# Kernel tuning notes

Measured on AMD Instinct MI355X. Metric: run time of the kernel, lower is better.

## Reference

```python
import jax, jax.numpy as jnp
import numpy as np

B, L, H, C = 1, 512, 1024, 2


def setup_inputs() -> dict:
    key = jax.random.key(0)
    k1, k2, k3 = jax.random.split(key, 3)
    lm_output = jax.random.normal(k1, (B, L, H), dtype=jnp.float32)
    # torch Linear weight layout: [out_features, in_features]
    W1 = jax.random.normal(k2, (H, 2 * H), dtype=jnp.float32) * 0.02
    b1 = jnp.zeros((H,), dtype=jnp.float32)
    W2 = jax.random.normal(k3, (C, H), dtype=jnp.float32) * 0.02
    b2 = jnp.zeros((C,), dtype=jnp.float32)
    return {"lm_output": lm_output, "W1": W1, "b1": b1, "W2": W2, "b2": b2}


def reference(lm_output, W1, b1, W2, b2):
    # pair_emb[b,i,j] = concat(lm_output[b,j], lm_output[b,i])
    # Linear(concat(a,b)) decomposes: split W1 into the halves acting on each part.
    Wa = W1[:, :H]  # acts on lm_output_a (the j / column token)
    Wb = W1[:, H:]  # acts on lm_output_b (the i / row token)
    a_proj = jnp.einsum('blh,oh->blo', lm_output, Wa)  # [B,L,H]
    b_proj = jnp.einsum('blh,oh->blo', lm_output, Wb)  # [B,L,H]
    # hidden[b,i,j] = tanh(a_proj[b,j] + b_proj[b,i] + b1)   -> [B,L,L,H]
    hidden = jnp.tanh(a_proj[:, None, :, :] + b_proj[:, :, None, :] + b1)
    # Dropout is identity at inference time.
    logits = jnp.einsum('bijh,ch->bijc', hidden, W2) + b2  # [B,L,L,C]
    logits = (logits + jnp.swapaxes(logits, 1, 2)) / 2.0
    return logits
```

## Files before the change

kernel.cpp:

```cpp
#include <hip/hip_runtime.h>
#include <hip/hip_bf16.h>

#define HH 1024
#define LL 512

typedef __attribute__((ext_vector_type(8))) short bf16x8;
typedef __attribute__((ext_vector_type(4))) float f32x4;

static constexpr float C_EXP = 2.8853900817779268f;

static __device__ __forceinline__ uint4 pack8(float4 a, float4 b) {
    union { uint4 u; __hip_bfloat162 h[4]; } r;
    r.h[0] = __float22bfloat162_rn(make_float2(a.x, a.y));
    r.h[1] = __float22bfloat162_rn(make_float2(a.z, a.w));
    r.h[2] = __float22bfloat162_rn(make_float2(b.x, b.y));
    r.h[3] = __float22bfloat162_rn(make_float2(b.z, b.w));
    return r.u;
}

__global__ __launch_bounds__(256) void proj_mfma_kernel(
    const float* __restrict__ lm, const float* __restrict__ W1,
    const float* __restrict__ b1, float* __restrict__ Ea, float* __restrict__ Eb)
{
    __shared__ ushort As[32][72];
    __shared__ ushort Bs[64][72];

    const int tid  = threadIdx.x;
    const int lane = tid & 63;
    const int w    = tid >> 6;
    const int mbase = blockIdx.y * 32;
    const int nbase = blockIdx.x * 64;
    const int wm = (w & 1) * 16;
    const int wn = (w >> 1) * 32;

    const int sel  = nbase >> 10;
    const int nrow = nbase & 1023;

    f32x4 acc0 = {0.f, 0.f, 0.f, 0.f};
    f32x4 acc1 = {0.f, 0.f, 0.f, 0.f};

    const int srow = tid >> 3;
    const int sc8  = (tid & 7) * 8;

    const int mrow = lane & 15;
    const int q8   = (lane >> 4) * 8;

    for (int kb = 0; kb < HH; kb += 64) {
        __syncthreads();
        {
            const float* pa = &lm[(mbase + srow) * HH + kb + sc8];
            *(uint4*)&As[srow][sc8] = pack8(*(const float4*)pa, *(const float4*)(pa + 4));
            const float* pb0 = &W1[(nrow + srow) * 2048 + sel * 1024 + kb + sc8];
            *(uint4*)&Bs[srow][sc8] = pack8(*(const float4*)pb0, *(const float4*)(pb0 + 4));
            const float* pb1 = &W1[(nrow + srow + 32) * 2048 + sel * 1024 + kb + sc8];
            *(uint4*)&Bs[srow + 32][sc8] = pack8(*(const float4*)pb1, *(const float4*)(pb1 + 4));
        }
        __syncthreads();

#pragma unroll
        for (int s = 0; s < 2; ++s) {
            const bf16x8 a  = *(const bf16x8*)&As[wm + mrow][s * 32 + q8];
            const bf16x8 b0 = *(const bf16x8*)&Bs[wn + mrow][s * 32 + q8];
            const bf16x8 bf = *(const bf16x8*)&Bs[wn + 16 + mrow][s * 32 + q8];
            acc0 = __builtin_amdgcn_mfma_f32_16x16x32_bf16(a, b0, acc0, 0, 0, 0);
            acc1 = __builtin_amdgcn_mfma_f32_16x16x32_bf16(a, bf, acc1, 0, 0, 0);
        }
    }

    const int col = lane & 15;
    const int rq  = (lane >> 4) * 4;
#pragma unroll
    for (int t = 0; t < 2; ++t) {
        const f32x4 acc = t ? acc1 : acc0;
        const int n_g = nbase + wn + t * 16 + col;
        const int m0  = mbase + wm + rq;
        if (n_g < HH) {
            const float bb = b1[n_g];
#pragma unroll
            for (int r = 0; r < 4; ++r)
                Ea[(m0 + r) * HH + n_g] = __builtin_amdgcn_exp2f(C_EXP * (acc[r] + bb));
        } else {
#pragma unroll
            for (int r = 0; r < 4; ++r)
                Eb[(m0 + r) * HH + (n_g - HH)] = __builtin_amdgcn_exp2f(C_EXP * acc[r]);
        }
    }
}

__global__ __launch_bounds__(256, 4) void pair_kernel(
    const float* __restrict__ Ea, const float* __restrict__ Eb,
    const float* __restrict__ W2, const float* __restrict__ b2,
    float* __restrict__ out)
{
    __shared__ float a_s[32][132];
    __shared__ float b_s[32][132];
    __shared__ float w0_s[256], w1_s[256];
    __shared__ float s_red[2];

    const int tid   = threadIdx.x;
    const int tx    = tid & 15;
    const int ty    = tid >> 4;
    const int jbase = blockIdx.x * 32;
    const int ibase = blockIdx.y * 32;
    const int k0    = blockIdx.z * 256;

    if (tid < 128) {
        const int c = tid >> 6, q = tid & 63;
        const float4 v = *(const float4*)&W2[c * HH + k0 + q * 4];
        ((float4*)(c ? w1_s : w0_s))[q] =
            make_float4(-2.f * v.x, -2.f * v.y, -2.f * v.z, -2.f * v.w);
    }
    if (tid < 128) {
        const int c = tid >> 6, l = tid & 63;
        const float* ws = c ? w1_s : w0_s;
        float s = ws[l] + ws[l + 64] + ws[l + 128] + ws[l + 192];
#pragma unroll
        for (int off = 32; off; off >>= 1) s += __shfl_down(s, off, 64);
        if (l == 0) s_red[c] = s;
    }

    float acc[2][2][2] = {};

    for (int kb = 0; kb < 256; kb += 128) {
        __syncthreads();
        int p = tid;
#pragma unroll
        for (int it = 0; it < 8; ++it, p += 256) {
            const int row = p >> 5;
            const int c4  = p & 31;
            if (row < 32)
                *(float4*)&a_s[row][c4 * 4] =
                    *(const float4*)&Ea[(jbase + row) * HH + k0 + kb + c4 * 4];
            else
                *(float4*)&b_s[row - 32][c4 * 4] =
                    *(const float4*)&Eb[(ibase + row - 32) * HH + k0 + kb + c4 * 4];
        }
        __syncthreads();

#pragma unroll 4
        for (int h4 = 0; h4 < 32; ++h4) {
            const float4 ea0 = *(const float4*)&a_s[tx][h4 * 4];
            const float4 ea1 = *(const float4*)&a_s[tx + 16][h4 * 4];
            const float4 eb0 = *(const float4*)&b_s[ty][h4 * 4];
            const float4 eb1 = *(const float4*)&b_s[ty + 16][h4 * 4];
            const float4 w0  = *(const float4*)&w0_s[kb + h4 * 4];
            const float4 w1  = *(const float4*)&w1_s[kb + h4 * 4];

#define DO_H(EA0, EA1, EB0, EB1, W0V, W1V)                            \
            {                                                         \
                const float d00 = __builtin_fmaf((EB0), (EA0), 1.f);  \
                const float d01 = __builtin_fmaf((EB0), (EA1), 1.f);  \
                const float d10 = __builtin_fmaf((EB1), (EA0), 1.f);  \
                const float d11 = __builtin_fmaf((EB1), (EA1), 1.f);  \
                const float p0 = d00 * d01, p1 = d10 * d11;           \
                const float R  = __builtin_amdgcn_rcpf(p0 * p1);      \
                const float q0 = R * p1, q1 = R * p0;                 \
                const float r00 = q0 * d01, r01 = q0 * d00;           \
                const float r10 = q1 * d11, r11 = q1 * d10;           \
                acc[0][0][0] = __builtin_fmaf(r00, (W0V), acc[0][0][0]); \
                acc[0][0][1] = __builtin_fmaf(r00, (W1V), acc[0][0][1]); \
                acc[0][1][0] = __builtin_fmaf(r01, (W0V), acc[0][1][0]); \
                acc[0][1][1] = __builtin_fmaf(r01, (W1V), acc[0][1][1]); \
                acc[1][0][0] = __builtin_fmaf(r10, (W0V), acc[1][0][0]); \
                acc[1][0][1] = __builtin_fmaf(r10, (W1V), acc[1][0][1]); \
                acc[1][1][0] = __builtin_fmaf(r11, (W0V), acc[1][1][0]); \
                acc[1][1][1] = __builtin_fmaf(r11, (W1V), acc[1][1][1]); \
            }
            DO_H(ea0.x, ea1.x, eb0.x, eb1.x, w0.x, w1.x)
            DO_H(ea0.y, ea1.y, eb0.y, eb1.y, w0.y, w1.y)
            DO_H(ea0.z, ea1.z, eb0.z, eb1.z, w0.z, w1.z)
            DO_H(ea0.w, ea1.w, eb0.w, eb1.w, w0.w, w1.w)
#undef DO_H
        }
    }

    const float sc0 = -0.25f * s_red[0];
    const float sc1 = -0.25f * s_red[1];
    const float bb0 = (blockIdx.z == 0) ? 0.5f * b2[0] : 0.f;
    const float bb1 = (blockIdx.z == 0) ? 0.5f * b2[1] : 0.f;

#pragma unroll
    for (int ii = 0; ii < 2; ++ii) {
#pragma unroll
        for (int jj = 0; jj < 2; ++jj) {
            const int i = ibase + ty + ii * 16;
            const int j = jbase + tx + jj * 16;
            const float v0 = 0.5f * acc[ii][jj][0] + sc0 + bb0;
            const float v1 = 0.5f * acc[ii][jj][1] + sc1 + bb1;
            atomicAdd(&out[(i * LL + j) * 2 + 0], v0);
            atomicAdd(&out[(i * LL + j) * 2 + 1], v1);
            atomicAdd(&out[(j * LL + i) * 2 + 0], v0);
            atomicAdd(&out[(j * LL + i) * 2 + 1], v1);
        }
    }
}

extern "C" void kernel_launch(void* const* d_in, const int* in_sizes, int n_in,
                              void* d_out, int out_size, void* d_ws, size_t ws_size,
                              hipStream_t stream)
{
    const float* lm = (const float*)d_in[0];
    const float* W1 = (const float*)d_in[1];
    const float* b1 = (const float*)d_in[2];
    const float* W2 = (const float*)d_in[3];
    const float* b2 = (const float*)d_in[4];
    float* out = (float*)d_out;

    float* Ea = (float*)d_ws;
    float* Eb = Ea + (size_t)LL * HH;

    hipMemsetAsync(d_out, 0, (size_t)LL * LL * 2 * sizeof(float), stream);
    proj_mfma_kernel<<<dim3(32, 16), 256, 0, stream>>>(lm, W1, b1, Ea, Eb);
    pair_kernel<<<dim3(16, 16, 4), 256, 0, stream>>>(Ea, Eb, W2, b2, out);
}
```

Baseline: 157.3 us.

## Exploit output symmetry with upper-triangle tiles and deterministic split-K combine

Result: faster. 137.1 us (-12.9%).

```diff
diff --git a/kernel.cpp b/kernel.cpp
--- a/kernel.cpp
+++ b/kernel.cpp
@@ -3,6 +3,8 @@
 
 #define HH 1024
 #define LL 512
+#define NT 16
+#define NTRI 136
 
 typedef __attribute__((ext_vector_type(8))) short bf16x8;
 typedef __attribute__((ext_vector_type(4))) float f32x4;
@@ -18,181 +20,220 @@
     return r.u;
 }
 
-__global__ __launch_bounds__(256) void proj_mfma_kernel(
+__global__ __launch_bounds__(256, 4) void proj_mfma_kernel(
     const float* __restrict__ lm, const float* __restrict__ W1,
     const float* __restrict__ b1, float* __restrict__ Ea, float* __restrict__ Eb)
 {
-    __shared__ ushort As[32][72];
-    __shared__ ushort Bs[64][72];
+    __shared__ ushort As[16][136];
+    __shared__ ushort Bs[64][136];
 
     const int tid  = threadIdx.x;
     const int lane = tid & 63;
     const int w    = tid >> 6;
-    const int mbase = blockIdx.y * 32;
+    const int mbase = blockIdx.y * 16;
     const int nbase = blockIdx.x * 64;
-    const int wm = (w & 1) * 16;
-    const int wn = (w >> 1) * 32;
-
     const int sel  = nbase >> 10;
     const int nrow = nbase & 1023;
-
-    f32x4 acc0 = {0.f, 0.f, 0.f, 0.f};
-    f32x4 acc1 = {0.f, 0.f, 0.f, 0.f};
-
-    const int srow = tid >> 3;
-    const int sc8  = (tid & 7) * 8;
+    const int wn   = w * 16;
 
     const int mrow = lane & 15;
     const int q8   = (lane >> 4) * 8;
 
-    for (int kb = 0; kb < HH; kb += 64) {
+    f32x4 acc = {0.f, 0.f, 0.f, 0.f};
+
+    for (int kb = 0; kb < HH; kb += 128) {
         __syncthreads();
         {
-            const float* pa = &lm[(mbase + srow) * HH + kb + sc8];
-            *(uint4*)&As[srow][sc8] = pack8(*(const float4*)pa, *(const float4*)(pa + 4));
-            const float* pb0 = &W1[(nrow + srow) * 2048 + sel * 1024 + kb + sc8];
-            *(uint4*)&Bs[srow][sc8] = pack8(*(const float4*)pb0, *(const float4*)(pb0 + 4));
-            const float* pb1 = &W1[(nrow + srow + 32) * 2048 + sel * 1024 + kb + sc8];
-            *(uint4*)&Bs[srow + 32][sc8] = pack8(*(const float4*)pb1, *(const float4*)(pb1 + 4));
-        }
-        __syncthreads();
-
-#pragma unroll
-        for (int s = 0; s < 2; ++s) {
-            const bf16x8 a  = *(const bf16x8*)&As[wm + mrow][s * 32 + q8];
-            const bf16x8 b0 = *(const bf16x8*)&Bs[wn + mrow][s * 32 + q8];
-            const bf16x8 bf = *(const bf16x8*)&Bs[wn + 16 + mrow][s * 32 + q8];
-            acc0 = __builtin_amdgcn_mfma_f32_16x16x32_bf16(a, b0, acc0, 0, 0, 0);
-            acc1 = __builtin_amdgcn_mfma_f32_16x16x32_bf16(a, bf, acc1, 0, 0, 0);
+            const int row = tid >> 4, c8 = (tid & 15) * 8;
+            const float* pa = &lm[(mbase + row) * HH + kb + c8];
+            *(uint4*)&As[row][c8] = pack8(*(const float4*)pa, *(const float4*)(pa + 4));
+            int p = tid;
+#pragma unroll
+            for (int it = 0; it < 4; ++it, p += 256) {
+                const int br = p >> 4, bc8 = (p & 15) * 8;
+                const float* pb = &W1[(nrow + br) * 2048 + sel * 1024 + kb + bc8];
+                *(uint4*)&Bs[br][bc8] = pack8(*(const float4*)pb, *(const float4*)(pb + 4));
+            }
+        }
+        __syncthreads();
+
+#pragma unroll
+        for (int s = 0; s < 4; ++s) {
+            const bf16x8 a = *(const bf16x8*)&As[mrow][s * 32 + q8];
+            const bf16x8 b = *(const bf16x8*)&Bs[wn + mrow][s * 32 + q8];
+            acc = __builtin_amdgcn_mfma_f32_16x16x32_bf16(a, b, acc, 0, 0, 0);
         }
     }
 
     const int col = lane & 15;
     const int rq  = (lane >> 4) * 4;
-#pragma unroll
-    for (int t = 0; t < 2; ++t) {
-        const f32x4 acc = t ? acc1 : acc0;
-        const int n_g = nbase + wn + t * 16 + col;
-        const int m0  = mbase + wm + rq;
-        if (n_g < HH) {
-            const float bb = b1[n_g];
-#pragma unroll
-            for (int r = 0; r < 4; ++r)
-                Ea[(m0 + r) * HH + n_g] = __builtin_amdgcn_exp2f(C_EXP * (acc[r] + bb));
-        } else {
-#pragma unroll
-            for (int r = 0; r < 4; ++r)
-                Eb[(m0 + r) * HH + (n_g - HH)] = __builtin_amdgcn_exp2f(C_EXP * acc[r]);
-        }
+    const int n_g = nbase + wn + col;
+    const int m0  = mbase + rq;
+    if (n_g < HH) {
+        const float bb = b1[n_g];
+#pragma unroll
+        for (int r = 0; r < 4; ++r)
+            Ea[(m0 + r) * HH + n_g] = __builtin_amdgcn_exp2f(C_EXP * (acc[r] + bb));
+    } else {
+#pragma unroll
+        for (int r = 0; r < 4; ++r)
+            Eb[(m0 + r) * HH + (n_g - HH)] = __builtin_amdgcn_exp2f(C_EXP * acc[r]);
     }
 }
 
 __global__ __launch_bounds__(256, 4) void pair_kernel(
     const float* __restrict__ Ea, const float* __restrict__ Eb,
-    const float* __restrict__ W2, const float* __restrict__ b2,
-    float* __restrict__ out)
-{
-    __shared__ float a_s[32][132];
-    __shared__ float b_s[32][132];
+    const float* __restrict__ W2, float* __restrict__ pbuf, int nz)
+{
+    __shared__ float eaj[32][68];
+    __shared__ float eai[32][68];
+    __shared__ float ebi[32][68];
+    __shared__ float ebj[32][68];
     __shared__ float w0_s[256], w1_s[256];
     __shared__ float s_red[2];
 
-    const int tid   = threadIdx.x;
-    const int tx    = tid & 15;
-    const int ty    = tid >> 4;
-    const int jbase = blockIdx.x * 32;
-    const int ibase = blockIdx.y * 32;
-    const int k0    = blockIdx.z * 256;
-
-    if (tid < 128) {
-        const int c = tid >> 6, q = tid & 63;
-        const float4 v = *(const float4*)&W2[c * HH + k0 + q * 4];
-        ((float4*)(c ? w1_s : w0_s))[q] =
-            make_float4(-2.f * v.x, -2.f * v.y, -2.f * v.z, -2.f * v.w);
-    }
+    const int tid = threadIdx.x;
+    const int tx  = tid & 15;
+    const int ty  = tid >> 4;
+
+    int tt = blockIdx.x, bi = 0, rem = NT;
+    while (tt >= rem) { tt -= rem; --rem; ++bi; }
+    const int bj    = bi + tt;
+    const int ibase = bi * 32;
+    const int jbase = bj * 32;
+    const int slice = HH / nz;
+    const int k0    = blockIdx.y * slice;
+
     if (tid < 128) {
         const int c = tid >> 6, l = tid & 63;
-        const float* ws = c ? w1_s : w0_s;
-        float s = ws[l] + ws[l + 64] + ws[l + 128] + ws[l + 192];
+        float* ws = c ? w1_s : w0_s;
+        float s = 0.f;
+        for (int q = l; q < slice / 4; q += 64) {
+            const float4 v = *(const float4*)&W2[c * HH + k0 + q * 4];
+            const float4 nv = make_float4(-2.f * v.x, -2.f * v.y, -2.f * v.z, -2.f * v.w);
+            ((float4*)ws)[q] = nv;
+            s += nv.x + nv.y + nv.z + nv.w;
+        }
 #pragma unroll
         for (int off = 32; off; off >>= 1) s += __shfl_down(s, off, 64);
-        if (l == 0) s_red[c] = s;
+        if (l == 0) s_red[c] = -0.5f * s;
     }
 
     float acc[2][2][2] = {};
 
-    for (int kb = 0; kb < 256; kb += 128) {
-        __syncthreads();
-        int p = tid;
-#pragma unroll
-        for (int it = 0; it < 8; ++it, p += 256) {
-            const int row = p >> 5;
-            const int c4  = p & 31;
-            if (row < 32)
-                *(float4*)&a_s[row][c4 * 4] =
-                    *(const float4*)&Ea[(jbase + row) * HH + k0 + kb + c4 * 4];
-            else
-                *(float4*)&b_s[row - 32][c4 * 4] =
-                    *(const float4*)&Eb[(ibase + row - 32) * HH + k0 + kb + c4 * 4];
+    for (int kb = 0; kb < slice; kb += 64) {
+        __syncthreads();
+        {
+            int p = tid;
+#pragma unroll
+            for (int it = 0; it < 8; ++it, p += 256) {
+                const int tile = p >> 9;
+                const int row  = (p >> 4) & 31;
+                const int c4   = p & 15;
+                float4 v;
+                if      (tile == 0) v = *(const float4*)&Ea[(jbase + row) * HH + k0 + kb + c4 * 4];
+                else if (tile == 1) v = *(const float4*)&Ea[(ibase + row) * HH + k0 + kb + c4 * 4];
+                else if (tile == 2) v = *(const float4*)&Eb[(ibase + row) * HH + k0 + kb + c4 * 4];
+                else                v = *(const float4*)&Eb[(jbase + row) * HH + k0 + kb + c4 * 4];
+                if      (tile == 0) *(float4*)&eaj[row][c4 * 4] = v;
+                else if (tile == 1) *(float4*)&eai[row][c4 * 4] = v;
+                else if (tile == 2) *(float4*)&ebi[row][c4 * 4] = v;
+                else                *(float4*)&ebj[row][c4 * 4] = v;
+            }
         }
         __syncthreads();
 
 #pragma unroll 4
-        for (int h4 = 0; h4 < 32; ++h4) {
-            const float4 ea0 = *(const float4*)&a_s[tx][h4 * 4];
-            const float4 ea1 = *(const float4*)&a_s[tx + 16][h4 * 4];
-            const float4 eb0 = *(const float4*)&b_s[ty][h4 * 4];
-            const float4 eb1 = *(const float4*)&b_s[ty + 16][h4 * 4];
+        for (int h4 = 0; h4 < 16; ++h4) {
+            const float4 Aj0 = *(const float4*)&eaj[tx][h4 * 4];
+            const float4 Aj1 = *(const float4*)&eaj[tx + 16][h4 * 4];
+            const float4 Bi0 = *(const float4*)&ebi[ty][h4 * 4];
+            const float4 Bi1 = *(const float4*)&ebi[ty + 16][h4 * 4];
+            const float4 Ai0 = *(const float4*)&eai[ty][h4 * 4];
+            const float4 Ai1 = *(const float4*)&eai[ty + 16][h4 * 4];
+            const float4 Bj0 = *(const float4*)&ebj[tx][h4 * 4];
+            const float4 Bj1 = *(const float4*)&ebj[tx + 16][h4 * 4];
             const float4 w0  = *(const float4*)&w0_s[kb + h4 * 4];
             const float4 w1  = *(const float4*)&w1_s[kb + h4 * 4];
 
-#define DO_H(EA0, EA1, EB0, EB1, W0V, W1V)                            \
-            {                                                         \
-                const float d00 = __builtin_fmaf((EB0), (EA0), 1.f);  \
-                const float d01 = __builtin_fmaf((EB0), (EA1), 1.f);  \
-                const float d10 = __builtin_fmaf((EB1), (EA0), 1.f);  \
-                const float d11 = __builtin_fmaf((EB1), (EA1), 1.f);  \
-                const float p0 = d00 * d01, p1 = d10 * d11;           \
-                const float R  = __builtin_amdgcn_rcpf(p0 * p1);      \
-                const float q0 = R * p1, q1 = R * p0;                 \
-                const float r00 = q0 * d01, r01 = q0 * d00;           \
-                const float r10 = q1 * d11, r11 = q1 * d10;           \
-                acc[0][0][0] = __builtin_fmaf(r00, (W0V), acc[0][0][0]); \
-                acc[0][0][1] = __builtin_fmaf(r00, (W1V), acc[0][0][1]); \
-                acc[0][1][0] = __builtin_fmaf(r01, (W0V), acc[0][1][0]); \
-                acc[0][1][1] = __builtin_fmaf(r01, (W1V), acc[0][1][1]); \
-                acc[1][0][0] = __builtin_fmaf(r10, (W0V), acc[1][0][0]); \
-                acc[1][0][1] = __builtin_fmaf(r10, (W1V), acc[1][0][1]); \
-                acc[1][1][0] = __builtin_fmaf(r11, (W0V), acc[1][1][0]); \
-                acc[1][1][1] = __builtin_fmaf(r11, (W1V), acc[1][1][1]); \
+#define DO_H(AJ0, AJ1, BI0, BI1, AI0, AI1, BJ0, BJ1, W0V, W1V)        \
+            {                                                          \
+                const float d00 = __builtin_fmaf((BI0), (AJ0), 1.f);   \
+                const float d01 = __builtin_fmaf((BI0), (AJ1), 1.f);   \
+                const float d10 = __builtin_fmaf((BI1), (AJ0), 1.f);   \
+                const float d11 = __builtin_fmaf((BI1), (AJ1), 1.f);   \
+                const float e00 = __builtin_fmaf((AI0), (BJ0), 1.f);   \
+                const float e01 = __builtin_fmaf((AI0), (BJ1), 1.f);   \
+                const float e10 = __builtin_fmaf((AI1), (BJ0), 1.f);   \
+                const float e11 = __builtin_fmaf((AI1), (BJ1), 1.f);   \
+                const float dp0 = d00 * d01, dp1 = d10 * d11;          \
+                const float DR  = __builtin_amdgcn_rcpf(dp0 * dp1);    \
+                const float dq0 = DR * dp1, dq1 = DR * dp0;            \
+                const float rd00 = dq0 * d01, rd01 = dq0 * d00;        \
+                const float rd10 = dq1 * d11, rd11 = dq1 * d10;        \
+                const float ep0 = e00 * e01, ep1 = e10 * e11;          \
+                const float ER  = __builtin_amdgcn_rcpf(ep0 * ep1);    \
+                const float eq0 = ER * ep1, eq1 = ER * ep0;            \
+                const float re00 = eq0 * e01, re01 = eq0 * e00;        \
+                const float re10 = eq1 * e11, re11 = eq1 * e10;        \
+                const float u00 = rd00 + re00, u01 = rd01 + re01;      \
+                const float u10 = rd10 + re10, u11 = rd11 + re11;      \
+                acc[0][0][0] = __builtin_fmaf(u00, (W0V), acc[0][0][0]); \
+                acc[0][0][1] = __builtin_fmaf(u00, (W1V), acc[0][0][1]); \
+                acc[0][1][0] = __builtin_fmaf(u01, (W0V), acc[0][1][0]); \
+                acc[0][1][1] = __builtin_fmaf(u01, (W1V), acc[0][1][1]); \
+                acc[1][0][0] = __builtin_fmaf(u10, (W0V), acc[1][0][0]); \
+                acc[1][0][1] = __builtin_fmaf(u10, (W1V), acc[1][0][1]); \
+                acc[1][1][0] = __builtin_fmaf(u11, (W0V), acc[1][1][0]); \
+                acc[1][1][1] = __builtin_fmaf(u11, (W1V), acc[1][1][1]); \
             }
-            DO_H(ea0.x, ea1.x, eb0.x, eb1.x, w0.x, w1.x)
-            DO_H(ea0.y, ea1.y, eb0.y, eb1.y, w0.y, w1.y)
-            DO_H(ea0.z, ea1.z, eb0.z, eb1.z, w0.z, w1.z)
-            DO_H(ea0.w, ea1.w, eb0.w, eb1.w, w0.w, w1.w)
+            DO_H(Aj0.x, Aj1.x, Bi0.x, Bi1.x, Ai0.x, Ai1.x, Bj0.x, Bj1.x, w0.x, w1.x)
+            DO_H(Aj0.y, Aj1.y, Bi0.y, Bi1.y, Ai0.y, Ai1.y, Bj0.y, Bj1.y, w0.y, w1.y)
+            DO_H(Aj0.z, Aj1.z, Bi0.z, Bi1.z, Ai0.z, Ai1.z, Bj0.z, Bj1.z, w0.z, w1.z)
+            DO_H(Aj0.w, Aj1.w, Bi0.w, Bi1.w, Ai0.w, Ai1.w, Bj0.w, Bj1.w, w0.w, w1.w)
 #undef DO_H
         }
     }
 
-    const float sc0 = -0.25f * s_red[0];
-    const float sc1 = -0.25f * s_red[1];
-    const float bb0 = (blockIdx.z == 0) ? 0.5f * b2[0] : 0.f;
-    const float bb1 = (blockIdx.z == 0) ? 0.5f * b2[1] : 0.f;
-
+    const float s0 = s_red[0];
+    const float s1 = s_red[1];
+    float* pb = pbuf + ((size_t)blockIdx.y * NTRI + blockIdx.x) * 2048;
 #pragma unroll
     for (int ii = 0; ii < 2; ++ii) {
 #pragma unroll
         for (int jj = 0; jj < 2; ++jj) {
-            const int i = ibase + ty + ii * 16;
-            const int j = jbase + tx + jj * 16;
-            const float v0 = 0.5f * acc[ii][jj][0] + sc0 + bb0;
-            const float v1 = 0.5f * acc[ii][jj][1] + sc1 + bb1;
-            atomicAdd(&out[(i * LL + j) * 2 + 0], v0);
-            atomicAdd(&out[(i * LL + j) * 2 + 1], v1);
-            atomicAdd(&out[(j * LL + i) * 2 + 0], v0);
-            atomicAdd(&out[(j * LL + i) * 2 + 1], v1);
-        }
-    }
+            const int li = ty + ii * 16, lj = tx + jj * 16;
+            float2* dst = (float2*)&pb[(li * 32 + lj) * 2];
+            *dst = make_float2(0.5f * acc[ii][jj][0] + s0,
+                               0.5f * acc[ii][jj][1] + s1);
+        }
+    }
+}
+
+__global__ __launch_bounds__(256) void combine_kernel(
+    const float* __restrict__ pbuf, const float* __restrict__ b2,
+    float* __restrict__ out, int nz)
+{
+    const int idx   = blockIdx.x * 256 + threadIdx.x;
+    const int t     = idx >> 11;
+    const int local = idx & 2047;
+    int tt = t, bi = 0, rem = NT;
+    while (tt >= rem) { tt -= rem; --rem; ++bi; }
+    const int bj = bi + tt;
+
+    float s = 0.f;
+    for (int z = 0; z < nz; ++z)
+        s += pbuf[((size_t)z * NTRI + t) * 2048 + local];
+
+    const int li = local >> 6;
+    const int lj = (local >> 1) & 31;
+    const int c  = local & 1;
+    s += b2[c];
+
+    const int i = bi * 32 + li;
+    const int j = bj * 32 + lj;
+    out[(i * LL + j) * 2 + c] = s;
+    out[(j * LL + i) * 2 + c] = s;
 }
 
 extern "C" void kernel_launch(void* const* d_in, const int* in_sizes, int n_in,
@@ -206,10 +247,15 @@
     const float* b2 = (const float*)d_in[4];
     float* out = (float*)d_out;
 
-    float* Ea = (float*)d_ws;
-    float* Eb = Ea + (size_t)LL * HH;
-
-    hipMemsetAsync(d_out, 0, (size_t)LL * LL * 2 * sizeof(float), stream);
-    proj_mfma_kernel<<<dim3(32, 16), 256, 0, stream>>>(lm, W1, b1, Ea, Eb);
-    pair_kernel<<<dim3(16, 16, 4), 256, 0, stream>>>(Ea, Eb, W2, b2, out);
-}
+    float* Ea   = (float*)d_ws;
+    float* Eb   = Ea + (size_t)LL * HH;
+    float* pbuf = Eb + (size_t)LL * HH;
+
+    const size_t base = (size_t)4 * LL * HH * 2;
+    int nz = 8;
+    while (nz > 1 && base + (size_t)nz * NTRI * 2048 * 4 > ws_size) nz >>= 1;
+
+    proj_mfma_kernel<<<dim3(32, 32), 256, 0, stream>>>(lm, W1, b1, Ea, Eb);
+    pair_kernel<<<dim3(NTRI, nz), 256, 0, stream>>>(Ea, Eb, W2, pbuf, nz);
+    combine_kernel<<<(NTRI * 2048) / 256, 256, 0, stream>>>(pbuf, b2, out, nz);
+}
```
